# Optimization experiments

Hardware: AMD Instinct MI355X
Metric: run time of the kernel (lower is better)

The kernel has to match this reference:

```python
import jax, jax.numpy as jnp
import numpy as np

NUM_HEADS = 16
NEG_INF = -2.0**32 + 1.0  # matches torch code's padding value
LN_EPS = 1e-5


def setup_inputs() -> dict:
    key = jax.random.key(0)
    ks = jax.random.split(key, 4)
    B, S, D = 8, 1024, 1024
    x = jax.random.normal(ks[0], (B, S, D), dtype=jnp.float32)
    W_qkv = jax.random.normal(ks[1], (D, 3 * D), dtype=jnp.float32) * 0.02
    b_qkv = jnp.zeros((3 * D,), dtype=jnp.float32)
    W_out = jax.random.normal(ks[2], (D, D), dtype=jnp.float32) * 0.02
    b_out = jnp.zeros((D,), dtype=jnp.float32)
    gamma = jnp.ones((D,), dtype=jnp.float32)
    beta = jnp.zeros((D,), dtype=jnp.float32)
    return {"x": x, "W_qkv": W_qkv, "b_qkv": b_qkv, "W_out": W_out,
            "b_out": b_out, "gamma": gamma, "beta": beta}


def reference(x, W_qkv, b_qkv, W_out, b_out, gamma, beta):
    B, S, D = x.shape
    H = NUM_HEADS
    hd = D // H
    # fused QKV projection
    qkv = x @ W_qkv + b_qkv                      # [B, S, 3D]
    q, k, v = jnp.split(qkv, 3, axis=-1)         # each [B, S, D]
    # split heads: chunk along feature dim == reshape to [B, H, S, hd]
    q = q.reshape(B, S, H, hd).transpose(0, 2, 1, 3)
    k = k.reshape(B, S, H, hd).transpose(0, 2, 1, 3)
    v = v.reshape(B, S, H, hd).transpose(0, 2, 1, 3)
    # NOTE: original scales by sqrt(num_units), not sqrt(head_dim)
    scale = jnp.float32(1.0 / (D ** 0.5))
    scores = jnp.einsum('bhqd,bhkd->bhqk', q, k) * scale   # [B, H, S, S]
    causal = jnp.tril(jnp.ones((S, S), dtype=bool))
    scores = jnp.where(causal, scores, jnp.float32(NEG_INF))
    attn = jax.nn.softmax(scores, axis=-1)
    o = jnp.einsum('bhqk,bhkd->bhqd', attn, v)             # [B, H, S, hd]
    o = o.transpose(0, 2, 1, 3).reshape(B, S, D)           # concat heads
    out = o @ W_out + b_out + x                            # proj + residual
    # LayerNorm over last dim
    mu = jnp.mean(out, axis=-1, keepdims=True)
    var = jnp.mean((out - mu) ** 2, axis=-1, keepdims=True)
    out = (out - mu) * jax.lax.rsqrt(var + LN_EPS) * gamma + beta
    return out
```

## Files before the change

### kernel.cpp

```cpp
#include <hip/hip_runtime.h>
#include <math.h>

typedef __attribute__((ext_vector_type(8))) short bf16x8;
typedef __attribute__((ext_vector_type(4))) float f32x4;

#define DEV __device__ __forceinline__

DEV unsigned short f2b(float f) {
    union { float f; unsigned u; } x;
    x.f = f;
    unsigned r = x.u + 0x7fff + ((x.u >> 16) & 1);
    return (unsigned short)(r >> 16);
}
DEV float b2f(unsigned short u) {
    union { unsigned u; float f; } x;
    x.u = ((unsigned)u) << 16;
    return x.f;
}

DEV void glds16(const void* g, void* l) {
    __builtin_amdgcn_global_load_lds(
        (const __attribute__((address_space(1))) void*)g,
        (__attribute__((address_space(3))) void*)l, 16, 0, 0);
}

__global__ __launch_bounds__(256) void cvt_bf16(
    const float* __restrict__ in, unsigned short* __restrict__ out)
{
    int i = (blockIdx.x * 256 + threadIdx.x) * 8;
    float4 a = *(const float4*)(in + i);
    float4 b = *(const float4*)(in + i + 4);
    int4 tv;
    short* tp = reinterpret_cast<short*>(&tv);
    tp[0] = (short)f2b(a.x); tp[1] = (short)f2b(a.y);
    tp[2] = (short)f2b(a.z); tp[3] = (short)f2b(a.w);
    tp[4] = (short)f2b(b.x); tp[5] = (short)f2b(b.y);
    tp[6] = (short)f2b(b.z); tp[7] = (short)f2b(b.w);
    *(int4*)(out + i) = tv;
}

__global__ __launch_bounds__(256) void transpose_cvt(
    const float* __restrict__ W, unsigned short* __restrict__ Wt, int N)
{
    __shared__ short S[64 * 65];
    const int n0 = blockIdx.x * 64, k0 = blockIdx.y * 64;
    const int tid = threadIdx.x;
#pragma unroll
    for (int p = 0; p < 16; p++) {
        int idx = p * 256 + tid;
        int r = idx >> 6, c = idx & 63;
        S[c * 65 + r] = (short)f2b(W[(size_t)(k0 + r) * N + n0 + c]);
    }
    __syncthreads();
#pragma unroll
    for (int p = 0; p < 8; p++) {
        int idx = p * 256 + tid;
        int r = idx >> 5, cp = (idx & 31) * 2;
        unsigned lo = (unsigned short)S[r * 65 + cp];
        unsigned hi = (unsigned short)S[r * 65 + cp + 1];
        *(unsigned*)(Wt + (size_t)(n0 + r) * 1024 + k0 + cp) = lo | (hi << 16);
    }
}

__global__ __launch_bounds__(256) void qkv_gemm(
    const unsigned short* __restrict__ Xb,
    const unsigned short* __restrict__ Wt,
    const float* __restrict__ bq,
    unsigned short* __restrict__ Qb,
    unsigned short* __restrict__ Kf,
    unsigned short* __restrict__ Vf)
{
    __shared__ __align__(16) short As[128 * 64];
    __shared__ __align__(16) short Bs[128 * 64];

    const int m0 = blockIdx.y * 128, n0 = blockIdx.x * 128;
    const int tid = threadIdx.x;
    const int wave = tid >> 6, lane = tid & 63;
    const int quad = lane >> 4, lcol = lane & 15;
    const int wrow = (wave >> 1) * 64, wcol = (wave & 1) * 64;

    f32x4 acc[4][4];
#pragma unroll
    for (int i = 0; i < 4; i++)
#pragma unroll
        for (int j = 0; j < 4; j++) acc[i][j] = (f32x4){0.f, 0.f, 0.f, 0.f};

    const int sr = tid >> 3;
    const int sc8 = (tid & 7) * 8;

    for (int k0 = 0; k0 < 1024; k0 += 64) {
        __syncthreads();
#pragma unroll
        for (int p = 0; p < 4; p++) {
            glds16(Xb + (size_t)(m0 + p * 32 + sr) * 1024 + k0 + sc8,
                   &As[(p * 32 + sr) * 64 + sc8]);
            glds16(Wt + (size_t)(n0 + p * 32 + sr) * 1024 + k0 + sc8,
                   &Bs[(p * 32 + sr) * 64 + sc8]);
        }
        __syncthreads();
#pragma unroll
        for (int kk = 0; kk < 2; kk++) {
            int ko = kk * 32 + quad * 8;
            bf16x8 a[4], b[4];
#pragma unroll
            for (int i = 0; i < 4; i++)
                a[i] = *(const bf16x8*)(&As[(wrow + 16 * i + lcol) * 64 + ko]);
#pragma unroll
            for (int j = 0; j < 4; j++)
                b[j] = *(const bf16x8*)(&Bs[(wcol + 16 * j + lcol) * 64 + ko]);
#pragma unroll
            for (int i = 0; i < 4; i++)
#pragma unroll
                for (int j = 0; j < 4; j++)
                    acc[i][j] = __builtin_amdgcn_mfma_f32_16x16x32_bf16(
                        a[i], b[j], acc[i][j], 0, 0, 0);
        }
    }

#pragma unroll
    for (int j = 0; j < 4; j++) {
        int cc = n0 + wcol + 16 * j + lcol;
        float bias = bq[cc];
        int which = cc >> 10, d = cc & 1023;
        int h = d >> 6, e = d & 63;
        if (which == 0) {
#pragma unroll
            for (int i = 0; i < 4; i++) {
#pragma unroll
                for (int reg = 0; reg < 4; reg++) {
                    int r = m0 + wrow + 16 * i + quad * 4 + reg;
                    int bb = r >> 10, s = r & 1023;
                    Qb[(size_t)((bb * 16 + h) * 1024 + s) * 64 + e] =
                        f2b(acc[i][j][reg] + bias);
                }
            }
        } else if (which == 1) {
            int kk_k = e >> 5, quad_k = (e >> 3) & 3, t_k = e & 7;
#pragma unroll
            for (int i = 0; i < 4; i++) {
#pragma unroll
                for (int reg = 0; reg < 4; reg++) {
                    int r = m0 + wrow + 16 * i + quad * 4 + reg;
                    int bb = r >> 10, s = r & 1023;
                    int kt_k = s >> 7, j_k = (s >> 4) & 7, lcol_k = s & 15;
                    size_t idx =
                        ((((size_t)(bb * 16 + h) * 8 + kt_k) * 2 + kk_k) * 8 + j_k) * 512
                        + (quad_k * 16 + lcol_k) * 8 + t_k;
                    Kf[idx] = f2b(acc[i][j][reg] + bias);
                }
            }
        } else {
            int jo_v = e >> 4, lcol_v = e & 15;
#pragma unroll
            for (int i = 0; i < 4; i++) {
                int r0 = m0 + wrow + 16 * i + quad * 4;
                int bb = r0 >> 10, s0 = r0 & 1023;
                int kt_v = s0 >> 7, kk2_v = (s0 >> 5) & 3;
                int quad_v = (s0 >> 3) & 3, t0 = s0 & 7;
                ushort4 pk;
                pk.x = f2b(acc[i][j][0] + bias);
                pk.y = f2b(acc[i][j][1] + bias);
                pk.z = f2b(acc[i][j][2] + bias);
                pk.w = f2b(acc[i][j][3] + bias);
                size_t base =
                    ((((size_t)(bb * 16 + h) * 8 + kt_v) * 4 + kk2_v) * 4 + jo_v) * 512
                    + (quad_v * 16 + lcol_v) * 8 + t0;
                *(ushort4*)(Vf + base) = pk;
            }
        }
    }
}

__global__ __launch_bounds__(256, 4) void attn_kern(
    const unsigned short* __restrict__ Qb,
    const unsigned short* __restrict__ Kf,
    const unsigned short* __restrict__ Vf,
    unsigned short* __restrict__ Ob)
{
    __shared__ __align__(16) short Ps[64 * 136];

    const int xb = blockIdx.x;
    const int bh = blockIdx.y;
    const int pr = xb >> 1;
    const int hf = xb & 1;
    const unsigned short* Qp = Qb + (size_t)bh * 65536;
    const unsigned short* Kp = Kf + (size_t)bh * 65536;
    const unsigned short* Vp = Vf + (size_t)bh * 65536;

    const int tid = threadIdx.x;
    const int wave = tid >> 6, lane = tid & 63;
    const int quad = lane >> 4, lcol = lane & 15;
    const int hw4 = hf * 4 + wave;
    const int qloc = hw4 * 16 + lcol;

    const float sc2 = 0.0450711882f;
    const int b = bh >> 4, h = bh & 15;

    for (int pass = 0; pass < 2; pass++) {
        const int qt = pass ? (7 - pr) : pr;
        const int q0 = qt * 128 + hf * 64 + wave * 16;

        bf16x8 qa[2];
#pragma unroll
        for (int kk = 0; kk < 2; kk++)
            qa[kk] = *(const bf16x8*)(Qp + (size_t)(q0 + lcol) * 64
                                      + kk * 32 + quad * 8);

        f32x4 o_acc[4];
#pragma unroll
        for (int jo = 0; jo < 4; jo++) o_acc[jo] = (f32x4){0.f, 0.f, 0.f, 0.f};
        float l_loc = 0.f;

        for (int kt = 0; kt <= qt; kt++) {
            const bool diag = (kt == qt);
            const int jmax = diag ? hw4 : 7;
            const int kk2max = diag ? (hw4 >> 1) : 3;

            f32x4 scT[8];
#pragma unroll
            for (int j = 0; j < 8; j++) scT[j] = (f32x4){0.f, 0.f, 0.f, 0.f};
#pragma unroll
            for (int kk = 0; kk < 2; kk++) {
                bf16x8 kb[8];
#pragma unroll
                for (int j = 0; j < 8; j++)
                    if (j <= jmax)
                        kb[j] = *(const bf16x8*)(Kp
                            + ((size_t)((kt * 2 + kk) * 8 + j) << 9) + lane * 8);
#pragma unroll
                for (int j = 0; j < 8; j++)
                    if (j <= jmax)
                        scT[j] = __builtin_amdgcn_mfma_f32_16x16x32_bf16(
                            kb[j], qa[kk], scT[j], 0, 0, 0);
            }

#pragma unroll
            for (int j = 0; j < 8; j++) {
                if (j <= jmax) {
                    float pv[4];
#pragma unroll
                    for (int r = 0; r < 4; r++) {
                        float p = exp2f(scT[j][r] * sc2);
                        if (diag && (16 * j + quad * 4 + r) > qloc) p = 0.f;
                        l_loc += p;
                        pv[r] = p;
                    }
                    ushort4 pk;
                    pk.x = f2b(pv[0]); pk.y = f2b(pv[1]);
                    pk.z = f2b(pv[2]); pk.w = f2b(pv[3]);
                    *(ushort4*)(&Ps[(wave * 16 + lcol) * 136 + 16 * j + quad * 4]) = pk;
                }
            }
            if (diag && !(jmax & 1)) {
                *(ushort4*)(&Ps[(wave * 16 + lcol) * 136 + 16 * (jmax + 1) + quad * 4]) =
                    (ushort4){0, 0, 0, 0};
            }

#pragma unroll
            for (int kk2 = 0; kk2 < 4; kk2++) {
                if (kk2 <= kk2max) {
                    bf16x8 pa = *(const bf16x8*)(&Ps[(wave * 16 + lcol) * 136
                                                     + kk2 * 32 + quad * 8]);
                    bf16x8 vb[4];
#pragma unroll
                    for (int jo = 0; jo < 4; jo++)
                        vb[jo] = *(const bf16x8*)(Vp
                            + ((size_t)((kt * 4 + kk2) * 4 + jo) << 9) + lane * 8);
#pragma unroll
                    for (int jo = 0; jo < 4; jo++)
                        o_acc[jo] = __builtin_amdgcn_mfma_f32_16x16x32_bf16(
                            pa, vb[jo], o_acc[jo], 0, 0, 0);
                }
            }
        }

        l_loc += __shfl_xor(l_loc, 16);
        l_loc += __shfl_xor(l_loc, 32);
        float inv = 1.0f / l_loc;
        float invq[4];
#pragma unroll
        for (int r = 0; r < 4; r++) invq[r] = __shfl(inv, quad * 4 + r);

#pragma unroll
        for (int jo = 0; jo < 4; jo++) {
#pragma unroll
            for (int r = 0; r < 4; r++) {
                int q = q0 + quad * 4 + r;
                Ob[(size_t)(b * 1024 + q) * 1024 + h * 64 + 16 * jo + lcol] =
                    f2b(o_acc[jo][r] * invq[r]);
            }
        }
        l_loc = 0.f;
    }
}

__global__ __launch_bounds__(256) void out_gemm(
    const unsigned short* __restrict__ O,
    const unsigned short* __restrict__ Wt2,
    const float* __restrict__ bo,
    const float* __restrict__ X,
    unsigned short* __restrict__ P2)
{
    __shared__ __align__(16) short As[128 * 64];
    __shared__ __align__(16) short Bs[128 * 64];

    const int m0 = blockIdx.y * 128, n0 = blockIdx.x * 128;
    const int tid = threadIdx.x;
    const int wave = tid >> 6, lane = tid & 63;
    const int quad = lane >> 4, lcol = lane & 15;
    const int wrow = (wave >> 1) * 64, wcol = (wave & 1) * 64;

    f32x4 acc[4][4];
#pragma unroll
    for (int i = 0; i < 4; i++)
#pragma unroll
        for (int j = 0; j < 4; j++) acc[i][j] = (f32x4){0.f, 0.f, 0.f, 0.f};

    const int sr = tid >> 3;
    const int sc8 = (tid & 7) * 8;

    for (int k0 = 0; k0 < 1024; k0 += 64) {
        __syncthreads();
#pragma unroll
        for (int p = 0; p < 4; p++) {
            glds16(O + (size_t)(m0 + p * 32 + sr) * 1024 + k0 + sc8,
                   &As[(p * 32 + sr) * 64 + sc8]);
            glds16(Wt2 + (size_t)(n0 + p * 32 + sr) * 1024 + k0 + sc8,
                   &Bs[(p * 32 + sr) * 64 + sc8]);
        }
        __syncthreads();
#pragma unroll
        for (int kk = 0; kk < 2; kk++) {
            int ko = kk * 32 + quad * 8;
            bf16x8 a[4], b[4];
#pragma unroll
            for (int i = 0; i < 4; i++)
                a[i] = *(const bf16x8*)(&As[(wrow + 16 * i + lcol) * 64 + ko]);
#pragma unroll
            for (int j = 0; j < 4; j++)
                b[j] = *(const bf16x8*)(&Bs[(wcol + 16 * j + lcol) * 64 + ko]);
#pragma unroll
            for (int i = 0; i < 4; i++)
#pragma unroll
                for (int j = 0; j < 4; j++)
                    acc[i][j] = __builtin_amdgcn_mfma_f32_16x16x32_bf16(
                        a[i], b[j], acc[i][j], 0, 0, 0);
        }
    }

#pragma unroll
    for (int j = 0; j < 4; j++) {
        int c = n0 + wcol + 16 * j + lcol;
        float bias = bo[c];
#pragma unroll
        for (int i = 0; i < 4; i++) {
#pragma unroll
            for (int reg = 0; reg < 4; reg++) {
                int r = m0 + wrow + 16 * i + quad * 4 + reg;
                float v = acc[i][j][reg] + bias + X[(size_t)r * 1024 + c];
                P2[(size_t)r * 1024 + c] = f2b(v);
            }
        }
    }
}

__global__ __launch_bounds__(256) void ln_kern(
    const unsigned short* __restrict__ P2,
    const float* __restrict__ G,
    const float* __restrict__ Bt,
    float* __restrict__ out)
{
    const int row = blockIdx.x, tid = threadIdx.x;
    const size_t base = (size_t)row * 1024 + tid * 4;

    int2 raw = *(const int2*)(P2 + base);
    float v[4];
    v[0] = b2f((unsigned short)(raw.x & 0xffff));
    v[1] = b2f((unsigned short)((unsigned)raw.x >> 16));
    v[2] = b2f((unsigned short)(raw.y & 0xffff));
    v[3] = b2f((unsigned short)((unsigned)raw.y >> 16));

    float sum = v[0] + v[1] + v[2] + v[3];
    float sq = v[0] * v[0] + v[1] * v[1] + v[2] * v[2] + v[3] * v[3];
#pragma unroll
    for (int m = 1; m < 64; m <<= 1) {
        sum += __shfl_xor(sum, m);
        sq += __shfl_xor(sq, m);
    }
    __shared__ float rs[4], rq[4];
    const int wave = tid >> 6, lane = tid & 63;
    if (lane == 0) { rs[wave] = sum; rq[wave] = sq; }
    __syncthreads();
    sum = rs[0] + rs[1] + rs[2] + rs[3];
    sq = rq[0] + rq[1] + rq[2] + rq[3];

    float mean = sum * (1.0f / 1024.0f);
    float var = fmaxf(sq * (1.0f / 1024.0f) - mean * mean, 0.0f);
    float rstd = rsqrtf(var + 1e-5f);

    float4 g = *(const float4*)(G + tid * 4);
    float4 be = *(const float4*)(Bt + tid * 4);

    float4 o;
    o.x = (v[0] - mean) * rstd * g.x + be.x;
    o.y = (v[1] - mean) * rstd * g.y + be.y;
    o.z = (v[2] - mean) * rstd * g.z + be.z;
    o.w = (v[3] - mean) * rstd * g.w + be.w;
    *(float4*)(out + base) = o;
}

extern "C" void kernel_launch(void* const* d_in, const int* in_sizes, int n_in,
                              void* d_out, int out_size, void* d_ws, size_t ws_size,
                              hipStream_t stream) {
    const float* x    = (const float*)d_in[0];
    const float* Wqkv = (const float*)d_in[1];
    const float* bqkv = (const float*)d_in[2];
    const float* Wout = (const float*)d_in[3];
    const float* bout = (const float*)d_in[4];
    const float* gam  = (const float*)d_in[5];
    const float* bet  = (const float*)d_in[6];
    float* out = (float*)d_out;

    char* ws = (char*)d_ws;
    const size_t MB = (size_t)1024 * 1024;

    unsigned short* Qb  = (unsigned short*)d_out;
    unsigned short* Ob  = (unsigned short*)d_out + 8388608;
    unsigned short* Kf  = (unsigned short*)(ws);
    unsigned short* Vf  = (unsigned short*)(ws + 16 * MB);
    unsigned short* Wt2 = (unsigned short*)(ws + 32 * MB);
    unsigned short* Xb  = (unsigned short*)(ws + 34 * MB);
    unsigned short* Wt  = (unsigned short*)(ws + 50 * MB);
    unsigned short* P2  = (unsigned short*)(ws + 34 * MB);

    cvt_bf16<<<4096, 256, 0, stream>>>(x, Xb);
    transpose_cvt<<<dim3(48, 16), 256, 0, stream>>>(Wqkv, Wt, 3072);
    transpose_cvt<<<dim3(16, 16), 256, 0, stream>>>(Wout, Wt2, 1024);
    qkv_gemm<<<dim3(24, 64), 256, 0, stream>>>(Xb, Wt, bqkv, Qb, Kf, Vf);
    attn_kern<<<dim3(8, 128), 256, 0, stream>>>(Qb, Kf, Vf, Ob);
    out_gemm<<<dim3(8, 64), 256, 0, stream>>>(Ob, Wt2, bout, x, P2);
    ln_kern<<<8192, 256, 0, stream>>>(P2, gam, bet, out);
}
```

Measured before the change: 279.4 us.

## Enlarge QKV GEMM tile, swizzle LDS, remap blocks per XCD, stage epilogue via LDS

The QKV GEMM moves to 512-thread blocks computing 256x128 tiles, which reuses each B tile across more rows. Block indices are remapped so that blocks on the same XCD share M rows, aiming for better L2 locality. Both GEMMs get an XOR swizzle on the LDS layout to cut bank conflicts on the MFMA operand reads. The QKV epilogue now writes the head-layout output into LDS first and then stores 16-byte vectors instead of scattered 2-byte stores. This costs extra syncs and LDS traffic, and the larger block may lower occupancy.

```diff
diff --git a/kernel.cpp b/kernel.cpp
--- a/kernel.cpp
+++ b/kernel.cpp
@@ -62,7 +62,7 @@
     }
 }
 
-__global__ __launch_bounds__(256) void qkv_gemm(
+__global__ __launch_bounds__(512, 4) void qkv_gemm(
     const unsigned short* __restrict__ Xb,
     const unsigned short* __restrict__ Wt,
     const float* __restrict__ bq,
@@ -70,14 +70,19 @@
     unsigned short* __restrict__ Kf,
     unsigned short* __restrict__ Vf)
 {
-    __shared__ __align__(16) short As[128 * 64];
+    __shared__ __align__(16) short As[256 * 64];
     __shared__ __align__(16) short Bs[128 * 64];
 
-    const int m0 = blockIdx.y * 128, n0 = blockIdx.x * 128;
+    const int flat = blockIdx.y * 24 + blockIdx.x;
+    const int xcd = flat & 7, local = flat >> 3;
+    const int m0 = (xcd * 4 + local / 24) * 256;
+    const int n0 = (local % 24) * 128;
+
     const int tid = threadIdx.x;
     const int wave = tid >> 6, lane = tid & 63;
     const int quad = lane >> 4, lcol = lane & 15;
-    const int wrow = (wave >> 1) * 64, wcol = (wave & 1) * 64;
+    const int wr = wave >> 1, wc = wave & 1;
+    const int wrow = wr * 64, wcol = wc * 64;
 
     f32x4 acc[4][4];
 #pragma unroll
@@ -86,28 +91,32 @@
         for (int j = 0; j < 4; j++) acc[i][j] = (f32x4){0.f, 0.f, 0.f, 0.f};
 
     const int sr = tid >> 3;
-    const int sc8 = (tid & 7) * 8;
+    const int g_lin = tid & 7;
+    const int g_src = g_lin ^ (sr & 7);
+    const int swz = lcol & 7;
 
     for (int k0 = 0; k0 < 1024; k0 += 64) {
         __syncthreads();
 #pragma unroll
-        for (int p = 0; p < 4; p++) {
-            glds16(Xb + (size_t)(m0 + p * 32 + sr) * 1024 + k0 + sc8,
-                   &As[(p * 32 + sr) * 64 + sc8]);
-            glds16(Wt + (size_t)(n0 + p * 32 + sr) * 1024 + k0 + sc8,
-                   &Bs[(p * 32 + sr) * 64 + sc8]);
-        }
+        for (int p = 0; p < 4; p++)
+            glds16(Xb + (size_t)(m0 + p * 64 + sr) * 1024 + k0 + g_src * 8,
+                   &As[(p * 64 + sr) * 64 + g_lin * 8]);
+#pragma unroll
+        for (int p = 0; p < 2; p++)
+            glds16(Wt + (size_t)(n0 + p * 64 + sr) * 1024 + k0 + g_src * 8,
+                   &Bs[(p * 64 + sr) * 64 + g_lin * 8]);
         __syncthreads();
 #pragma unroll
         for (int kk = 0; kk < 2; kk++) {
-            int ko = kk * 32 + quad * 8;
             bf16x8 a[4], b[4];
 #pragma unroll
             for (int i = 0; i < 4; i++)
-                a[i] = *(const bf16x8*)(&As[(wrow + 16 * i + lcol) * 64 + ko]);
+                a[i] = *(const bf16x8*)(&As[(wrow + 16 * i + lcol) * 64
+                                            + ((kk * 4 + quad) ^ swz) * 8]);
 #pragma unroll
             for (int j = 0; j < 4; j++)
-                b[j] = *(const bf16x8*)(&Bs[(wcol + 16 * j + lcol) * 64 + ko]);
+                b[j] = *(const bf16x8*)(&Bs[(wcol + 16 * j + lcol) * 64
+                                            + ((kk * 4 + quad) ^ swz) * 8]);
 #pragma unroll
             for (int i = 0; i < 4; i++)
 #pragma unroll
@@ -116,58 +125,58 @@
                         a[i], b[j], acc[i][j], 0, 0, 0);
         }
     }
-
-#pragma unroll
-    for (int j = 0; j < 4; j++) {
-        int cc = n0 + wcol + 16 * j + lcol;
-        float bias = bq[cc];
-        int which = cc >> 10, d = cc & 1023;
-        int h = d >> 6, e = d & 63;
-        if (which == 0) {
-#pragma unroll
-            for (int i = 0; i < 4; i++) {
-#pragma unroll
-                for (int reg = 0; reg < 4; reg++) {
-                    int r = m0 + wrow + 16 * i + quad * 4 + reg;
-                    int bb = r >> 10, s = r & 1023;
-                    Qb[(size_t)((bb * 16 + h) * 1024 + s) * 64 + e] =
-                        f2b(acc[i][j][reg] + bias);
+    __syncthreads();
+
+    short* Es = As;
+    const int which = n0 >> 10;
+    const int h0 = (n0 & 1023) >> 6;
+    const int bb = m0 >> 10;
+    const int sl0 = m0 & 1023;
+
+#pragma unroll
+    for (int hh = 0; hh < 2; hh++) {
+        if ((wr >> 1) == hh) {
+#pragma unroll
+            for (int j = 0; j < 4; j++) {
+                int colt = wcol + 16 * j + lcol;
+                float bias = bq[n0 + colt];
+                int g = colt >> 6, e = colt & 63;
+#pragma unroll
+                for (int i = 0; i < 4; i++) {
+#pragma unroll
+                    for (int reg = 0; reg < 4; reg++) {
+                        int ls = (wr & 1) * 64 + 16 * i + quad * 4 + reg;
+                        unsigned short v = f2b(acc[i][j][reg] + bias);
+                        int off;
+                        if (which == 0)
+                            off = ls * 64 + e;
+                        else if (which == 1)
+                            off = (e >> 5) * 4096 + (ls >> 4) * 512
+                                + (((e >> 3) & 3) * 16 + (ls & 15)) * 8 + (e & 7);
+                        else
+                            off = (ls >> 5) * 2048 + (e >> 4) * 512
+                                + ((((ls >> 3) & 3) * 16) + (e & 15)) * 8 + (ls & 7);
+                        Es[g * 8192 + off] = (short)v;
+                    }
                 }
             }
-        } else if (which == 1) {
-            int kk_k = e >> 5, quad_k = (e >> 3) & 3, t_k = e & 7;
-#pragma unroll
-            for (int i = 0; i < 4; i++) {
-#pragma unroll
-                for (int reg = 0; reg < 4; reg++) {
-                    int r = m0 + wrow + 16 * i + quad * 4 + reg;
-                    int bb = r >> 10, s = r & 1023;
-                    int kt_k = s >> 7, j_k = (s >> 4) & 7, lcol_k = s & 15;
-                    size_t idx =
-                        ((((size_t)(bb * 16 + h) * 8 + kt_k) * 2 + kk_k) * 8 + j_k) * 512
-                        + (quad_k * 16 + lcol_k) * 8 + t_k;
-                    Kf[idx] = f2b(acc[i][j][reg] + bias);
-                }
-            }
-        } else {
-            int jo_v = e >> 4, lcol_v = e & 15;
-#pragma unroll
-            for (int i = 0; i < 4; i++) {
-                int r0 = m0 + wrow + 16 * i + quad * 4;
-                int bb = r0 >> 10, s0 = r0 & 1023;
-                int kt_v = s0 >> 7, kk2_v = (s0 >> 5) & 3;
-                int quad_v = (s0 >> 3) & 3, t0 = s0 & 7;
-                ushort4 pk;
-                pk.x = f2b(acc[i][j][0] + bias);
-                pk.y = f2b(acc[i][j][1] + bias);
-                pk.z = f2b(acc[i][j][2] + bias);
-                pk.w = f2b(acc[i][j][3] + bias);
-                size_t base =
-                    ((((size_t)(bb * 16 + h) * 8 + kt_v) * 4 + kk2_v) * 4 + jo_v) * 512
-                    + (quad_v * 16 + lcol_v) * 8 + t0;
-                *(ushort4*)(Vf + base) = pk;
-            }
-        }
+        }
+        __syncthreads();
+        const int kt = (sl0 >> 7) + hh;
+#pragma unroll
+        for (int rd = 0; rd < 4; rd++) {
+            int fl = rd * 4096 + tid * 8;
+            int g = fl >> 13, off = fl & 8191;
+            bf16x8 val = *(const bf16x8*)(&Es[fl]);
+            int bh = bb * 16 + h0 + g;
+            if (which == 0)
+                *(bf16x8*)(Qb + ((size_t)bh * 1024 + sl0 + hh * 128) * 64 + off) = val;
+            else if (which == 1)
+                *(bf16x8*)(Kf + ((size_t)bh * 8 + kt) * 8192 + off) = val;
+            else
+                *(bf16x8*)(Vf + ((size_t)bh * 8 + kt) * 8192 + off) = val;
+        }
+        if (hh == 0) __syncthreads();
     }
 }
 
@@ -304,7 +313,11 @@
     __shared__ __align__(16) short As[128 * 64];
     __shared__ __align__(16) short Bs[128 * 64];
 
-    const int m0 = blockIdx.y * 128, n0 = blockIdx.x * 128;
+    const int flat = blockIdx.y * 8 + blockIdx.x;
+    const int xcd = flat & 7, local = flat >> 3;
+    const int m0 = (xcd * 8 + (local >> 3)) * 128;
+    const int n0 = (local & 7) * 128;
+
     const int tid = threadIdx.x;
     const int wave = tid >> 6, lane = tid & 63;
     const int quad = lane >> 4, lcol = lane & 15;
@@ -317,28 +330,31 @@
         for (int j = 0; j < 4; j++) acc[i][j] = (f32x4){0.f, 0.f, 0.f, 0.f};
 
     const int sr = tid >> 3;
-    const int sc8 = (tid & 7) * 8;
+    const int g_lin = tid & 7;
+    const int g_src = g_lin ^ (sr & 7);
+    const int swz = lcol & 7;
 
     for (int k0 = 0; k0 < 1024; k0 += 64) {
         __syncthreads();
 #pragma unroll
         for (int p = 0; p < 4; p++) {
-            glds16(O + (size_t)(m0 + p * 32 + sr) * 1024 + k0 + sc8,
-                   &As[(p * 32 + sr) * 64 + sc8]);
-            glds16(Wt2 + (size_t)(n0 + p * 32 + sr) * 1024 + k0 + sc8,
-                   &Bs[(p * 32 + sr) * 64 + sc8]);
+            glds16(O + (size_t)(m0 + p * 32 + sr) * 1024 + k0 + g_src * 8,
+                   &As[(p * 32 + sr) * 64 + g_lin * 8]);
+            glds16(Wt2 + (size_t)(n0 + p * 32 + sr) * 1024 + k0 + g_src * 8,
+                   &Bs[(p * 32 + sr) * 64 + g_lin * 8]);
         }
         __syncthreads();
 #pragma unroll
         for (int kk = 0; kk < 2; kk++) {
-            int ko = kk * 32 + quad * 8;
             bf16x8 a[4], b[4];
 #pragma unroll
             for (int i = 0; i < 4; i++)
-                a[i] = *(const bf16x8*)(&As[(wrow + 16 * i + lcol) * 64 + ko]);
+                a[i] = *(const bf16x8*)(&As[(wrow + 16 * i + lcol) * 64
+                                            + ((kk * 4 + quad) ^ swz) * 8]);
 #pragma unroll
             for (int j = 0; j < 4; j++)
-                b[j] = *(const bf16x8*)(&Bs[(wcol + 16 * j + lcol) * 64 + ko]);
+                b[j] = *(const bf16x8*)(&Bs[(wcol + 16 * j + lcol) * 64
+                                            + ((kk * 4 + quad) ^ swz) * 8]);
 #pragma unroll
             for (int i = 0; i < 4; i++)
 #pragma unroll
@@ -436,7 +452,7 @@
     cvt_bf16<<<4096, 256, 0, stream>>>(x, Xb);
     transpose_cvt<<<dim3(48, 16), 256, 0, stream>>>(Wqkv, Wt, 3072);
     transpose_cvt<<<dim3(16, 16), 256, 0, stream>>>(Wout, Wt2, 1024);
-    qkv_gemm<<<dim3(24, 64), 256, 0, stream>>>(Xb, Wt, bqkv, Qb, Kf, Vf);
+    qkv_gemm<<<dim3(24, 32), 512, 0, stream>>>(Xb, Wt, bqkv, Qb, Kf, Vf);
     attn_kern<<<dim3(8, 128), 256, 0, stream>>>(Qb, Kf, Vf, Ob);
     out_gemm<<<dim3(8, 64), 256, 0, stream>>>(Ob, Wt2, bout, x, P2);
     ln_kern<<<8192, 256, 0, stream>>>(P2, gam, bet, out);
```

Result: slower. 292.0 us (+4.5%).
